# Kernel tuning notes

Measured on AMD Instinct MI355X. Metric: run time of the kernel, lower is better.

Reference implementation:

```python
import jax, jax.numpy as jnp
import numpy as np


def swish(x):
    return x * jax.nn.sigmoid(x)


def setup_inputs() -> dict:
    key = jax.random.key(0)
    ks = jax.random.split(key, 12)
    b, n, c, h, dg, hid = 4, 512, 256, 8, 6, 16

    def lin(k, i, o):
        return jax.random.normal(k, (i, o), jnp.float32) / np.float32(np.sqrt(i))

    return {
        "pairwise_g": jax.random.normal(ks[0], (b, n, n, dg), jnp.float32),
        "coset_functions": jax.random.normal(ks[1], (b, n, c), jnp.float32),
        "fc_q_w": lin(ks[2], c, c), "fc_q_b": jnp.zeros((c,), jnp.float32),
        "fc_k_w": lin(ks[3], c, c), "fc_k_b": jnp.zeros((c,), jnp.float32),
        "in_w": lin(ks[4], c, c), "in_b": jnp.zeros((c,), jnp.float32),
        "out_w": lin(ks[5], c, c), "out_b": jnp.zeros((c,), jnp.float32),
        "loc_w1": jax.random.normal(ks[6], (h, dg, hid), jnp.float32) / np.float32(np.sqrt(dg)),
        "loc_b1": jnp.zeros((h, hid), jnp.float32),
        "loc_w2": jax.random.normal(ks[7], (h, hid, hid), jnp.float32) / np.float32(np.sqrt(hid)),
        "loc_b2": jnp.zeros((h, hid), jnp.float32),
        "loc_w3": jax.random.normal(ks[8], (h, hid, 1), jnp.float32) / np.float32(np.sqrt(hid)),
        "loc_b3": jnp.zeros((h, 1), jnp.float32),
        "mask": jax.random.randint(ks[9], (4, 512), 0, 2) > 0,
    }


def reference(pairwise_g, coset_functions, fc_q_w, fc_q_b, fc_k_w, fc_k_b,
              in_w, in_b, out_w, out_b,
              loc_w1, loc_b1, loc_w2, loc_b2, loc_w3, loc_b3, mask):
    # nbhd_idx = arange(n) in the original (dense neighborhoods), so all
    # advanced-index gathers are identities and are expressed as broadcasts.
    b, n, c = coset_functions.shape
    h = loc_w1.shape[0]
    d = c // h

    # DotProductKernel: scores scaled by sqrt(embed_dim) = sqrt(c)
    Q = (coset_functions @ fc_q_w + fc_q_b).reshape(b, n, h, d)
    K = (coset_functions @ fc_k_w + fc_k_b).reshape(b, n, h, d)
    A_feat = jnp.einsum('bnhd,bmhd->bnmh', Q, K) / np.float32(np.sqrt(c))  # (b,n,m,h)

    # MultiheadWeightNet location kernel: per-head 3-layer MLP with swish
    # after every linear (LieConv-style LinearBNact blocks), out_dim=1.
    x = swish(jnp.einsum('bnmg,hgk->bnmhk', pairwise_g, loc_w1) + loc_b1)
    x = swish(jnp.einsum('bnmhk,hkj->bnmhj', x, loc_w2) + loc_b2)
    A_loc = swish(jnp.einsum('bnmhk,hko->bnmho', x, loc_w3) + loc_b3)[..., 0]  # (b,n,m,h)

    pre = A_loc + A_feat
    nbhd_mask = mask[:, None, :, None]          # mask over keys j: (b,1,m,1)
    pre = jnp.where(nbhd_mask, pre, jnp.float32(-1e38))
    att = jax.nn.softmax(pre, axis=2)           # softmax over neighbor dim m

    V = (coset_functions @ in_w + in_b).reshape(b, n, h, d)  # input_linear
    out = jnp.einsum('bnmh,bmhd->bnhd', att, V).reshape(b, n, c)
    return out @ out_w + out_b                  # output_linear; (b,n,c_out)
```

## Files before the change

kernel.cpp:

```cpp
#include <hip/hip_runtime.h>
#include <math.h>

namespace {

constexpr int kB = 4, kN = 512, kC = 256, kH = 8, kDG = 6, kHID = 16;

constexpr int S_QH = 20;
constexpr int S_BT = 20;
constexpr int S_AT = 516;

typedef _Float16 half2v __attribute__((ext_vector_type(2)));
typedef _Float16 half4v __attribute__((ext_vector_type(4)));
typedef float float4v __attribute__((ext_vector_type(4)));
typedef unsigned uint2v __attribute__((ext_vector_type(2)));

__device__ __forceinline__ float swishf(float x) {
    return x * __builtin_amdgcn_rcpf(1.0f + __expf(-x));
}

__device__ __forceinline__ unsigned pk16(float a, float b) {
    unsigned short ha = __builtin_bit_cast(unsigned short, (_Float16)a);
    unsigned short hb = __builtin_bit_cast(unsigned short, (_Float16)b);
    return (unsigned)ha | ((unsigned)hb << 16);
}

__device__ __forceinline__ unsigned pkrtz(float a, float b) {
    return __builtin_bit_cast(unsigned, __builtin_amdgcn_cvt_pkrtz(a, b));
}

__device__ __forceinline__ float4v mfma16(half4v a, half4v b, float4v c) {
    return __builtin_amdgcn_mfma_f32_16x16x16f16(a, b, c, 0, 0, 0);
}

__global__ __launch_bounds__(256) void k_qkvc(
    const float* __restrict__ x,
    const float* __restrict__ wq, const float* __restrict__ bq,
    const float* __restrict__ wk, const float* __restrict__ bk,
    const float* __restrict__ wv, const float* __restrict__ bv,
    unsigned* __restrict__ Qh, unsigned* __restrict__ Kh,
    unsigned* __restrict__ Vh,
    const unsigned char* __restrict__ mraw,
    int* __restrict__ list, int* __restrict__ meta) {
    const int t = threadIdx.x;

    if (blockIdx.x == 512) {
        __shared__ int s_isbool;
        if (t == 0) s_isbool = 0;
        __syncthreads();
        int found = 0;
        for (int i = t; i < kB * kN; i += 256)
            if ((i & 3) && mraw[i]) found = 1;
        if (found) atomicOr(&s_isbool, 1);
        __syncthreads();
        const int isb = s_isbool;
        const int b = t >> 6, lane = t & 63;
        const int* mi = (const int*)mraw;
        int base = 0;
        for (int c = 0; c < 8; ++c) {
            const int m = c * 64 + lane;
            const int idx = b * kN + m;
            const int valid = isb ? (mraw[idx] != 0) : (mi[idx] != 0);
            unsigned long long bal = __ballot(valid);
            int rank = (int)__popcll(bal & ((1ull << lane) - 1ull));
            if (valid) list[b * kN + base + rank] = m;
            base += (int)__popcll(bal);
        }
        for (int i = base + lane; i < kN; i += 64)
            list[b * kN + i] = (base == 0) ? i : 0;
        if (lane == 0) {
            meta[b] = (base == 0) ? kN : base;
            meta[4 + b] = (base == 0);
        }
        return;
    }

    __shared__ float sx[8][kC];
    const int r0 = (blockIdx.x >> 1) * 8;
    const int c0 = (blockIdx.x & 1) * 128;
    const int col = t & 127;
    const int g = t >> 7;
    #pragma unroll
    for (int r = 0; r < 8; ++r) sx[r][t] = x[(r0 + r) * kC + t];
    __syncthreads();
    float aq[4] = {}, ak[4] = {}, av[4] = {};
    for (int k = 0; k < kC; ++k) {
        const float q = wq[k * kC + c0 + col];
        const float kk = wk[k * kC + c0 + col];
        const float v = wv[k * kC + c0 + col];
        #pragma unroll
        for (int r = 0; r < 4; ++r) {
            const float xs = sx[g * 4 + r][k];
            aq[r] += xs * q;
            ak[r] += xs * kk;
            av[r] += xs * v;
        }
    }
    const float qb = bq[c0 + col], kb = bk[c0 + col], vb = bv[c0 + col];
    #pragma unroll
    for (int r = 0; r < 4; ++r) {
        const int row = r0 + g * 4 + r;
        const float qv = aq[r] + qb;
        const float kv = ak[r] + kb;
        const float vv = av[r] + vb;
        const float qn = __shfl_down(qv, 1);
        const float kn = __shfl_down(kv, 1);
        const float vn = __shfl_down(vv, 1);
        if ((t & 1) == 0) {
            const int ci = (c0 + col) >> 1;
            Qh[row * (kC / 2) + ci] = pk16(qv, qn);
            Kh[row * (kC / 2) + ci] = pk16(kv, kn);
            Vh[row * (kC / 2) + ci] = pk16(vv, vn);
        }
    }
}

__global__ __launch_bounds__(256, 4) void k_attn(
    const float* __restrict__ G,
    const unsigned* __restrict__ Qh,
    const unsigned* __restrict__ Kh,
    const unsigned* __restrict__ Vh,
    const float* __restrict__ w1, const float* __restrict__ b1,
    const float* __restrict__ w2, const float* __restrict__ b2,
    const float* __restrict__ w3, const float* __restrict__ b3,
    const int* __restrict__ list, const int* __restrict__ meta,
    float* __restrict__ out) {
    __shared__ __align__(16) unsigned sQh[kH * S_QH];
    __shared__ __align__(16) uint4 sG4[kN];
    __shared__ int sList[kN];
    __shared__ __align__(16) float sB1T[kH * S_BT];
    __shared__ __align__(16) float sB2T[kH * S_BT];
    __shared__ __align__(16) float sW3T[kH * S_BT];
    __shared__ float sB3[kH];
    __shared__ float sAtt[kH * S_AT];
    __shared__ float sInv[kH];

    const int bn = blockIdx.x;
    const int b = bn >> 9;
    const int t = threadIdx.x;
    const int l = t & 63;
    const int p = l & 15;
    const int s = l >> 4;
    const int wid = t >> 6;

    half4v a1f[kH], a2f[kH];
    #pragma unroll
    for (int h = 0; h < kH; ++h) {
        #pragma unroll
        for (int r = 0; r < 4; ++r) {
            const int k = 4 * s + r;
            a1f[h][r] = (k < kDG) ? (_Float16)w1[(h * kDG + k) * kHID + p]
                                  : (_Float16)0.f;
            a2f[h][r] = (_Float16)w2[(h * kHID + k) * kHID + p];
        }
    }

    if (t < kH * S_QH) {
        const int hh = t / S_QH, r = t % S_QH;
        sQh[t] = (r < 16) ? Qh[bn * (kC / 2) + hh * 16 + r] : 0u;
    }
    sList[t] = list[b * kN + t];
    sList[t + 256] = list[b * kN + t + 256];
    #pragma unroll 1
    for (int rep = 0; rep < 2; ++rep) {
        const int m = t + rep * 256;
        const float* gp = G + ((size_t)bn * kN + m) * kDG;
        uint4 gw;
        gw.x = pkrtz(gp[0], gp[1]);
        gw.y = pkrtz(gp[2], gp[3]);
        gw.z = pkrtz(gp[4], gp[5]);
        gw.w = 0;
        sG4[m] = gw;
    }
    if (t < 128) {
        const int hh = t >> 4, j = t & 15;
        sB1T[hh * S_BT + j] = b1[hh * kHID + j];
        sB2T[hh * S_BT + j] = b2[hh * kHID + j];
        sW3T[hh * S_BT + j] = w3[hh * kHID + j];
        if (j == 0) sB3[hh] = b3[hh];
    }
    const int nv = meta[b];
    const int allm = meta[4 + b];
    __syncthreads();

    const unsigned* khB = Kh + (size_t)(b * kN) * (kC / 2);
    const int ntiles = (nv + 15) >> 4;

    #pragma unroll
    for (int h = 0; h < kH; ++h) {
        const float4v bv1 = *(const float4v*)&sB1T[h * S_BT + s * 4];
        const float4v bv2 = *(const float4v*)&sB2T[h * S_BT + s * 4];
        const float4v w3f = *(const float4v*)&sW3T[h * S_BT + s * 4];
        half4v w3h;
        #pragma unroll
        for (int r = 0; r < 4; ++r) w3h[r] = (_Float16)w3f[r];
        const float b3s = sB3[h];
        const float4v b3v = {b3s, b3s, b3s, b3s};
        const uint2v q0u = {sQh[h * S_QH + 2 * s], sQh[h * S_QH + 2 * s + 1]};
        const uint2v q1u = {sQh[h * S_QH + 8 + 2 * s], sQh[h * S_QH + 9 + 2 * s]};
        const half4v qA0 = __builtin_bit_cast(half4v, q0u);
        const half4v qA1 = __builtin_bit_cast(half4v, q1u);

        #pragma unroll 1
        for (int tile = wid; tile < ntiles; tile += 8) {
            const int mcwA = tile * 16 + p;
            const int mcwB = mcwA + 64;
            const int mcA = min(mcwA, nv - 1);
            const int mcB = min(mcwB, nv - 1);
            const int mA = sList[mcA];
            const int mB = sList[mcB];
            const unsigned* krA = khB + (size_t)mA * (kC / 2) + h * 16 + 2 * s;
            const unsigned* krB = khB + (size_t)mB * (kC / 2) + h * 16 + 2 * s;
            const uint2v k0A = {krA[0], krA[1]};
            const uint2v k1A = {krA[8], krA[9]};
            const uint2v k0B = {krB[0], krB[1]};
            const uint2v k1B = {krB[8], krB[9]};
            const unsigned* gpA = (const unsigned*)&sG4[mA];
            const unsigned* gpB = (const unsigned*)&sG4[mB];
            uint2v guA = {gpA[(s & 1) * 2], gpA[(s & 1) * 2 + 1]};
            uint2v guB = {gpB[(s & 1) * 2], gpB[(s & 1) * 2 + 1]};
            if (s >= 2) { guA[0] = 0u; guA[1] = 0u; guB[0] = 0u; guB[1] = 0u; }
            const half4v bgA = __builtin_bit_cast(half4v, guA);
            const half4v bgB = __builtin_bit_cast(half4v, guB);
            float4v caA = {0.f, 0.f, 0.f, 0.f};
            float4v caB = {0.f, 0.f, 0.f, 0.f};
            caA = mfma16(qA0, __builtin_bit_cast(half4v, k0A), caA);
            caB = mfma16(qA0, __builtin_bit_cast(half4v, k0B), caB);
            caA = mfma16(qA1, __builtin_bit_cast(half4v, k1A), caA);
            caB = mfma16(qA1, __builtin_bit_cast(half4v, k1B), caB);
            const float4v c1A = mfma16(a1f[h], bgA, bv1);
            const float4v c1B = mfma16(a1f[h], bgB, bv1);
            const uint2v x1uA = {pkrtz(swishf(c1A[0]), swishf(c1A[1])),
                                 pkrtz(swishf(c1A[2]), swishf(c1A[3]))};
            const uint2v x1uB = {pkrtz(swishf(c1B[0]), swishf(c1B[1])),
                                 pkrtz(swishf(c1B[2]), swishf(c1B[3]))};
            const float4v c2A = mfma16(a2f[h], __builtin_bit_cast(half4v, x1uA), bv2);
            const float4v c2B = mfma16(a2f[h], __builtin_bit_cast(half4v, x1uB), bv2);
            const uint2v x2uA = {pkrtz(swishf(c2A[0]), swishf(c2A[1])),
                                 pkrtz(swishf(c2A[2]), swishf(c2A[3]))};
            const uint2v x2uB = {pkrtz(swishf(c2B[0]), swishf(c2B[1])),
                                 pkrtz(swishf(c2B[2]), swishf(c2B[3]))};
            const float4v c3A = mfma16(w3h, __builtin_bit_cast(half4v, x2uA), b3v);
            const float4v c3B = mfma16(w3h, __builtin_bit_cast(half4v, x2uB), b3v);
            const float preA = swishf(c3A[0]) + caA[0] * 0.0625f;
            const float preB = swishf(c3B[0]) + caB[0] * 0.0625f;
            if (s == 0 && mcwA < nv) sAtt[h * S_AT + mcwA] = allm ? 0.f : preA;
            if (s == 0 && mcwB < nv) sAtt[h * S_AT + mcwB] = allm ? 0.f : preB;
        }
    }
    __syncthreads();

    {
        const int hg = t >> 5;
        const int lane = t & 31;
        float mx = -3.4e38f;
        for (int idx = lane; idx < nv; idx += 32)
            mx = fmaxf(mx, sAtt[hg * S_AT + idx]);
        #pragma unroll
        for (int off = 16; off; off >>= 1)
            mx = fmaxf(mx, __shfl_xor(mx, off));
        float ls = 0.f;
        for (int idx = lane; idx < nv; idx += 32) {
            const float e = __expf(sAtt[hg * S_AT + idx] - mx);
            sAtt[hg * S_AT + idx] = e;
            ls += e;
        }
        #pragma unroll
        for (int off = 16; off; off >>= 1)
            ls += __shfl_xor(ls, off);
        if (lane == 0) sInv[hg] = 1.0f / ls;
    }
    __syncthreads();

    {
        const int hg = t >> 5;
        const int dp = (t >> 1) & 15;
        const int par = t & 1;
        const unsigned* vbp = Vh + (size_t)(b * kN) * (kC / 2) + hg * 16 + dp;
        float alo = 0.f, ahi = 0.f, blo = 0.f, bhi = 0.f;
        int mc = par;
        for (; mc + 2 < nv; mc += 4) {
            const float aw0 = sAtt[hg * S_AT + mc];
            const float aw1 = sAtt[hg * S_AT + mc + 2];
            const half2v v0 = __builtin_bit_cast(half2v, vbp[(size_t)sList[mc] * (kC / 2)]);
            const half2v v1 = __builtin_bit_cast(half2v, vbp[(size_t)sList[mc + 2] * (kC / 2)]);
            alo += aw0 * (float)v0[0];
            ahi += aw0 * (float)v0[1];
            blo += aw1 * (float)v1[0];
            bhi += aw1 * (float)v1[1];
        }
        for (; mc < nv; mc += 2) {
            const float aw = sAtt[hg * S_AT + mc];
            const half2v vv = __builtin_bit_cast(half2v, vbp[(size_t)sList[mc] * (kC / 2)]);
            alo += aw * (float)vv[0];
            ahi += aw * (float)vv[1];
        }
        alo += blo; ahi += bhi;
        alo += __shfl_xor(alo, 1);
        ahi += __shfl_xor(ahi, 1);
        out[bn * kC + t] = (par ? ahi : alo) * sInv[hg];
    }
}

__global__ __launch_bounds__(256) void k_proj(
    const float* __restrict__ x,
    const float* __restrict__ w, const float* __restrict__ bias,
    float* __restrict__ y) {
    __shared__ float sx[8][kC];
    const int t = threadIdx.x;
    const int r0 = (blockIdx.x >> 1) * 8;
    const int c0 = (blockIdx.x & 1) * 128;
    const int col = t & 127;
    const int g = t >> 7;
    #pragma unroll
    for (int r = 0; r < 8; ++r) sx[r][t] = x[(r0 + r) * kC + t];
    __syncthreads();
    float acc[4] = {};
    for (int k = 0; k < kC; ++k) {
        const float wv = w[k * kC + c0 + col];
        #pragma unroll
        for (int r = 0; r < 4; ++r) acc[r] += sx[g * 4 + r][k] * wv;
    }
    const float bb = bias[c0 + col];
    #pragma unroll
    for (int r = 0; r < 4; ++r)
        y[(r0 + g * 4 + r) * kC + c0 + col] = acc[r] + bb;
}

}

extern "C" void kernel_launch(void* const* d_in, const int* in_sizes, int n_in,
                              void* d_out, int out_size, void* d_ws, size_t ws_size,
                              hipStream_t stream) {
    (void)in_sizes; (void)n_in; (void)out_size; (void)ws_size;
    const float* G  = (const float*)d_in[0];
    const float* cf = (const float*)d_in[1];
    const float* wq = (const float*)d_in[2];
    const float* bq = (const float*)d_in[3];
    const float* wk = (const float*)d_in[4];
    const float* bk = (const float*)d_in[5];
    const float* wv = (const float*)d_in[6];
    const float* bv = (const float*)d_in[7];
    const float* wo = (const float*)d_in[8];
    const float* bo = (const float*)d_in[9];
    const float* w1 = (const float*)d_in[10];
    const float* b1 = (const float*)d_in[11];
    const float* w2 = (const float*)d_in[12];
    const float* b2 = (const float*)d_in[13];
    const float* w3 = (const float*)d_in[14];
    const float* b3 = (const float*)d_in[15];
    const unsigned char* mraw = (const unsigned char*)d_in[16];

    const int rows = kB * kN;
    unsigned* Qh = (unsigned*)d_ws;
    unsigned* Kh = Qh + (size_t)rows * (kC / 2);
    unsigned* Vh = Kh + (size_t)rows * (kC / 2);
    float* O = (float*)(Vh + (size_t)rows * (kC / 2));
    int* list = (int*)(O + (size_t)rows * kC);
    int* meta = list + rows;

    k_qkvc<<<513, 256, 0, stream>>>(cf, wq, bq, wk, bk, wv, bv,
                                    Qh, Kh, Vh, mraw, list, meta);
    k_attn<<<rows, 256, 0, stream>>>(G, Qh, Kh, Vh, w1, b1, w2, b2, w3, b3,
                                     list, meta, O);
    k_proj<<<512, 256, 0, stream>>>(O, wo, bo, (float*)d_out);
}
```

Before: 268.8 us.

## Split attention into tiled logits kernel and separate softmax/value kernel

Replaces the per-query-row attention kernel with a 16x16 (query, key) tiled logits kernel that computes the QK dot products and the location MLP, then writes fp16 logits to a workspace buffer. A new softmax kernel reads those logits back and does the softmax and the value aggregation. This improves reuse of K/Q and gives more parallelism per block, at the cost of an extra global round trip for an fp16 logits tensor and fp16 rounding of the pre-softmax values. It also adds unroll pragmas to the projection loops.

```diff
diff --git a/kernel.cpp b/kernel.cpp
--- a/kernel.cpp
+++ b/kernel.cpp
@@ -5,13 +5,15 @@
 
 constexpr int kB = 4, kN = 512, kC = 256, kH = 8, kDG = 6, kHID = 16;
 
-constexpr int S_QH = 20;
 constexpr int S_BT = 20;
 constexpr int S_AT = 516;
+constexpr int S_G  = 10;
+constexpr int S_L  = 18;
 
 typedef _Float16 half2v __attribute__((ext_vector_type(2)));
 typedef _Float16 half4v __attribute__((ext_vector_type(4)));
 typedef float float4v __attribute__((ext_vector_type(4)));
+typedef float float2v __attribute__((ext_vector_type(2)));
 typedef unsigned uint2v __attribute__((ext_vector_type(2)));
 
 __device__ __forceinline__ float swishf(float x) {
@@ -83,6 +85,7 @@
     for (int r = 0; r < 8; ++r) sx[r][t] = x[(r0 + r) * kC + t];
     __syncthreads();
     float aq[4] = {}, ak[4] = {}, av[4] = {};
+    #pragma unroll 4
     for (int k = 0; k < kC; ++k) {
         const float q = wq[k * kC + c0 + col];
         const float kk = wk[k * kC + c0 + col];
@@ -114,28 +117,33 @@
     }
 }
 
-__global__ __launch_bounds__(256, 4) void k_attn(
+__global__ __launch_bounds__(256, 4) void k_logits(
     const float* __restrict__ G,
     const unsigned* __restrict__ Qh,
     const unsigned* __restrict__ Kh,
-    const unsigned* __restrict__ Vh,
     const float* __restrict__ w1, const float* __restrict__ b1,
     const float* __restrict__ w2, const float* __restrict__ b2,
     const float* __restrict__ w3, const float* __restrict__ b3,
     const int* __restrict__ list, const int* __restrict__ meta,
-    float* __restrict__ out) {
-    __shared__ __align__(16) unsigned sQh[kH * S_QH];
-    __shared__ __align__(16) uint4 sG4[kN];
-    __shared__ int sList[kN];
+    unsigned* __restrict__ Ap) {
+    __shared__ __align__(16) unsigned sG[256 * S_G];
+    __shared__ __align__(16) float sL[128 * S_L];
     __shared__ __align__(16) float sB1T[kH * S_BT];
     __shared__ __align__(16) float sB2T[kH * S_BT];
     __shared__ __align__(16) float sW3T[kH * S_BT];
     __shared__ float sB3[kH];
-    __shared__ float sAtt[kH * S_AT];
-    __shared__ float sInv[kH];
-
-    const int bn = blockIdx.x;
-    const int b = bn >> 9;
+
+    const int bid = blockIdx.x;
+    const int b = bid >> 10;
+    const int rem = bid & 1023;
+    const int mtile = rem >> 5;
+    const int ntile = rem & 31;
+    const int nv = meta[b];
+    if (mtile * 16 >= nv) return;
+    const int allm = meta[4 + b];
+    const int n0 = ntile * 16;
+    const int m0c = mtile * 16;
+
     const int t = threadIdx.x;
     const int l = t & 63;
     const int p = l & 15;
@@ -152,24 +160,6 @@
                                   : (_Float16)0.f;
             a2f[h][r] = (_Float16)w2[(h * kHID + k) * kHID + p];
         }
-    }
-
-    if (t < kH * S_QH) {
-        const int hh = t / S_QH, r = t % S_QH;
-        sQh[t] = (r < 16) ? Qh[bn * (kC / 2) + hh * 16 + r] : 0u;
-    }
-    sList[t] = list[b * kN + t];
-    sList[t + 256] = list[b * kN + t + 256];
-    #pragma unroll 1
-    for (int rep = 0; rep < 2; ++rep) {
-        const int m = t + rep * 256;
-        const float* gp = G + ((size_t)bn * kN + m) * kDG;
-        uint4 gw;
-        gw.x = pkrtz(gp[0], gp[1]);
-        gw.y = pkrtz(gp[2], gp[3]);
-        gw.z = pkrtz(gp[4], gp[5]);
-        gw.w = 0;
-        sG4[m] = gw;
     }
     if (t < 128) {
         const int hh = t >> 4, j = t & 15;
@@ -178,74 +168,111 @@
         sW3T[hh * S_BT + j] = w3[hh * kHID + j];
         if (j == 0) sB3[hh] = b3[hh];
     }
+    {
+        const int m = list[b * kN + m0c + (t & 15)];
+        const int n = n0 + (t >> 4);
+        const float* gp = G + ((size_t)(b * kN + n) * kN + m) * kDG;
+        unsigned* d = &sG[t * S_G];
+        d[0] = pkrtz(gp[0], gp[1]);
+        d[1] = pkrtz(gp[2], gp[3]);
+        d[2] = pkrtz(gp[4], gp[5]);
+        d[3] = 0; d[4] = 0; d[5] = 0; d[6] = 0; d[7] = 0;
+    }
+    __syncthreads();
+
+    {
+        const int m = list[b * kN + m0c + p];
+        const unsigned* krow = Kh + (size_t)(b * kN + m) * (kC / 2);
+        const unsigned* qrow = Qh + (size_t)(b * kN + n0 + p) * (kC / 2);
+        #pragma unroll
+        for (int hh = 0; hh < 2; ++hh) {
+            const int h = wid * 2 + hh;
+            const uint2v k0 = *(const uint2v*)&krow[h * 16 + 2 * s];
+            const uint2v q0 = *(const uint2v*)&qrow[h * 16 + 2 * s];
+            const uint2v k1 = *(const uint2v*)&krow[h * 16 + 8 + 2 * s];
+            const uint2v q1 = *(const uint2v*)&qrow[h * 16 + 8 + 2 * s];
+            float4v c = {0.f, 0.f, 0.f, 0.f};
+            c = mfma16(__builtin_bit_cast(half4v, k0),
+                       __builtin_bit_cast(half4v, q0), c);
+            c = mfma16(__builtin_bit_cast(half4v, k1),
+                       __builtin_bit_cast(half4v, q1), c);
+            const int base = (p * kH + h) * S_L + 4 * s;
+            float2v lo = {c[0] * 0.0625f, c[1] * 0.0625f};
+            float2v hi = {c[2] * 0.0625f, c[3] * 0.0625f};
+            *(float2v*)&sL[base] = lo;
+            *(float2v*)&sL[base + 2] = hi;
+        }
+    }
+    __syncthreads();
+
+    #pragma unroll 1
+    for (int ni = 0; ni < 4; ++ni) {
+        const int nl = wid * 4 + ni;
+        const uint2v gu = *(const uint2v*)&sG[(nl * 16 + p) * S_G + 2 * s];
+        const half4v bg = __builtin_bit_cast(half4v, gu);
+        #pragma unroll
+        for (int h = 0; h < kH; ++h) {
+            const float4v bv1 = *(const float4v*)&sB1T[h * S_BT + s * 4];
+            const float4v bv2 = *(const float4v*)&sB2T[h * S_BT + s * 4];
+            const float4v w3f = *(const float4v*)&sW3T[h * S_BT + s * 4];
+            half4v w3h;
+            #pragma unroll
+            for (int r = 0; r < 4; ++r) w3h[r] = (_Float16)w3f[r];
+            const float b3s = sB3[h];
+            const float4v b3v = {b3s, b3s, b3s, b3s};
+            const float4v c1 = mfma16(a1f[h], bg, bv1);
+            const uint2v x1u = {pkrtz(swishf(c1[0]), swishf(c1[1])),
+                                pkrtz(swishf(c1[2]), swishf(c1[3]))};
+            const float4v c2 = mfma16(a2f[h], __builtin_bit_cast(half4v, x1u), bv2);
+            const uint2v x2u = {pkrtz(swishf(c2[0]), swishf(c2[1])),
+                                pkrtz(swishf(c2[2]), swishf(c2[3]))};
+            const float4v c3 = mfma16(w3h, __builtin_bit_cast(half4v, x2u), b3v);
+            if (s == 0) {
+                const int idx = (nl * kH + h) * S_L + p;
+                sL[idx] = allm ? 0.f : (swishf(c3[0]) + sL[idx]);
+            }
+        }
+    }
+    __syncthreads();
+
+    {
+        const int row = t >> 1, half = t & 1;
+        const int nl = row >> 3, h = row & 7;
+        const float* src = &sL[row * S_L + half * 8];
+        uint4 w;
+        w.x = pkrtz(src[0], src[1]);
+        w.y = pkrtz(src[2], src[3]);
+        w.z = pkrtz(src[4], src[5]);
+        w.w = pkrtz(src[6], src[7]);
+        unsigned* dst = Ap + ((size_t)(b * kN + n0 + nl) * kH + h) * (kN / 2)
+                        + mtile * 8 + half * 4;
+        *(uint4*)dst = w;
+    }
+}
+
+__global__ __launch_bounds__(256, 8) void k_soft(
+    const unsigned* __restrict__ Ap,
+    const unsigned* __restrict__ Vh,
+    const int* __restrict__ list, const int* __restrict__ meta,
+    float* __restrict__ out) {
+    __shared__ float sAtt[kH * S_AT];
+    __shared__ int sList[kN];
+    __shared__ float sInv[kH];
+
+    const int bn = blockIdx.x;
+    const int b = bn >> 9;
+    const int t = threadIdx.x;
     const int nv = meta[b];
-    const int allm = meta[4 + b];
-    __syncthreads();
-
-    const unsigned* khB = Kh + (size_t)(b * kN) * (kC / 2);
-    const int ntiles = (nv + 15) >> 4;
-
-    #pragma unroll
-    for (int h = 0; h < kH; ++h) {
-        const float4v bv1 = *(const float4v*)&sB1T[h * S_BT + s * 4];
-        const float4v bv2 = *(const float4v*)&sB2T[h * S_BT + s * 4];
-        const float4v w3f = *(const float4v*)&sW3T[h * S_BT + s * 4];
-        half4v w3h;
-        #pragma unroll
-        for (int r = 0; r < 4; ++r) w3h[r] = (_Float16)w3f[r];
-        const float b3s = sB3[h];
-        const float4v b3v = {b3s, b3s, b3s, b3s};
-        const uint2v q0u = {sQh[h * S_QH + 2 * s], sQh[h * S_QH + 2 * s + 1]};
-        const uint2v q1u = {sQh[h * S_QH + 8 + 2 * s], sQh[h * S_QH + 9 + 2 * s]};
-        const half4v qA0 = __builtin_bit_cast(half4v, q0u);
-        const half4v qA1 = __builtin_bit_cast(half4v, q1u);
-
-        #pragma unroll 1
-        for (int tile = wid; tile < ntiles; tile += 8) {
-            const int mcwA = tile * 16 + p;
-            const int mcwB = mcwA + 64;
-            const int mcA = min(mcwA, nv - 1);
-            const int mcB = min(mcwB, nv - 1);
-            const int mA = sList[mcA];
-            const int mB = sList[mcB];
-            const unsigned* krA = khB + (size_t)mA * (kC / 2) + h * 16 + 2 * s;
-            const unsigned* krB = khB + (size_t)mB * (kC / 2) + h * 16 + 2 * s;
-            const uint2v k0A = {krA[0], krA[1]};
-            const uint2v k1A = {krA[8], krA[9]};
-            const uint2v k0B = {krB[0], krB[1]};
-            const uint2v k1B = {krB[8], krB[9]};
-            const unsigned* gpA = (const unsigned*)&sG4[mA];
-            const unsigned* gpB = (const unsigned*)&sG4[mB];
-            uint2v guA = {gpA[(s & 1) * 2], gpA[(s & 1) * 2 + 1]};
-            uint2v guB = {gpB[(s & 1) * 2], gpB[(s & 1) * 2 + 1]};
-            if (s >= 2) { guA[0] = 0u; guA[1] = 0u; guB[0] = 0u; guB[1] = 0u; }
-            const half4v bgA = __builtin_bit_cast(half4v, guA);
-            const half4v bgB = __builtin_bit_cast(half4v, guB);
-            float4v caA = {0.f, 0.f, 0.f, 0.f};
-            float4v caB = {0.f, 0.f, 0.f, 0.f};
-            caA = mfma16(qA0, __builtin_bit_cast(half4v, k0A), caA);
-            caB = mfma16(qA0, __builtin_bit_cast(half4v, k0B), caB);
-            caA = mfma16(qA1, __builtin_bit_cast(half4v, k1A), caA);
-            caB = mfma16(qA1, __builtin_bit_cast(half4v, k1B), caB);
-            const float4v c1A = mfma16(a1f[h], bgA, bv1);
-            const float4v c1B = mfma16(a1f[h], bgB, bv1);
-            const uint2v x1uA = {pkrtz(swishf(c1A[0]), swishf(c1A[1])),
-                                 pkrtz(swishf(c1A[2]), swishf(c1A[3]))};
-            const uint2v x1uB = {pkrtz(swishf(c1B[0]), swishf(c1B[1])),
-                                 pkrtz(swishf(c1B[2]), swishf(c1B[3]))};
-            const float4v c2A = mfma16(a2f[h], __builtin_bit_cast(half4v, x1uA), bv2);
-            const float4v c2B = mfma16(a2f[h], __builtin_bit_cast(half4v, x1uB), bv2);
-            const uint2v x2uA = {pkrtz(swishf(c2A[0]), swishf(c2A[1])),
-                                 pkrtz(swishf(c2A[2]), swishf(c2A[3]))};
-            const uint2v x2uB = {pkrtz(swishf(c2B[0]), swishf(c2B[1])),
-                                 pkrtz(swishf(c2B[2]), swishf(c2B[3]))};
-            const float4v c3A = mfma16(w3h, __builtin_bit_cast(half4v, x2uA), b3v);
-            const float4v c3B = mfma16(w3h, __builtin_bit_cast(half4v, x2uB), b3v);
-            const float preA = swishf(c3A[0]) + caA[0] * 0.0625f;
-            const float preB = swishf(c3B[0]) + caB[0] * 0.0625f;
-            if (s == 0 && mcwA < nv) sAtt[h * S_AT + mcwA] = allm ? 0.f : preA;
-            if (s == 0 && mcwB < nv) sAtt[h * S_AT + mcwB] = allm ? 0.f : preB;
-        }
+
+    sList[t] = list[b * kN + t];
+    sList[t + 256] = list[b * kN + t + 256];
+    const unsigned* arow = Ap + (size_t)bn * kH * (kN / 2);
+    #pragma unroll
+    for (int rep = 0; rep < 8; ++rep) {
+        const unsigned val = arow[rep * 256 + t];
+        const half2v hv = __builtin_bit_cast(half2v, val);
+        float2v f = {(float)hv[0], (float)hv[1]};
+        *(float2v*)&sAtt[rep * S_AT + 2 * t] = f;
     }
     __syncthreads();
 
@@ -315,6 +342,7 @@
     for (int r = 0; r < 8; ++r) sx[r][t] = x[(r0 + r) * kC + t];
     __syncthreads();
     float acc[4] = {};
+    #pragma unroll 4
     for (int k = 0; k < kC; ++k) {
         const float wv = w[k * kC + c0 + col];
         #pragma unroll
@@ -355,12 +383,14 @@
     unsigned* Kh = Qh + (size_t)rows * (kC / 2);
     unsigned* Vh = Kh + (size_t)rows * (kC / 2);
     float* O = (float*)(Vh + (size_t)rows * (kC / 2));
-    int* list = (int*)(O + (size_t)rows * kC);
+    unsigned* Ap = (unsigned*)(O + (size_t)rows * kC);
+    int* list = (int*)(Ap + (size_t)rows * kH * (kN / 2));
     int* meta = list + rows;
 
     k_qkvc<<<513, 256, 0, stream>>>(cf, wq, bq, wk, bk, wv, bv,
                                     Qh, Kh, Vh, mraw, list, meta);
-    k_attn<<<rows, 256, 0, stream>>>(G, Qh, Kh, Vh, w1, b1, w2, b2, w3, b3,
-                                     list, meta, O);
+    k_logits<<<4096, 256, 0, stream>>>(G, Qh, Kh, w1, b1, w2, b2, w3, b3,
+                                       list, meta, Ap);
+    k_soft<<<rows, 256, 0, stream>>>(Ap, Vh, list, meta, O);
     k_proj<<<512, 256, 0, stream>>>(O, wo, bo, (float*)d_out);
 }
```

Measured after the change: 277.3 us. +3.2%, slower.
